# Kernel tuning notes

Measured on AMD Instinct MI355X. Metric: run time of the kernel, lower is better.

The kernel has to match this reference:

```python
import jax, jax.numpy as jnp
import numpy as np

B, L, D, NL, VOCAB = 2, 8192, 512, 8, 32
FFT_LEN = 2 * L  # causal linear conv via zero-padded FFT


def layernorm(x, g, b, eps=1e-5):
    mu = jnp.mean(x, axis=-1, keepdims=True)
    var = jnp.var(x, axis=-1, keepdims=True)
    return (x - mu) * jax.lax.rsqrt(var + eps) * g + b


def fftconv(v, h, bias):
    # v: [B, d, L], h: [d, L] long implicit filter, bias: [d] skip (the Hyena 'D' term)
    vf = jnp.fft.rfft(v, n=FFT_LEN)
    hf = jnp.fft.rfft(h, n=FFT_LEN)
    y = jnp.fft.irfft(vf * hf[None], n=FFT_LEN)[..., :L]
    return y + v * bias[:, None]


def short_conv(p, w, b):
    # causal depthwise conv, kernel size 3: p [B, C, L], w [C, 3], b [C]
    pp = jnp.pad(p, ((0, 0), (0, 0), (2, 0)))
    out = jax.lax.conv_general_dilated(pp, w[:, None, :], (1,), 'VALID',
                                       feature_group_count=p.shape[1])
    return out + b[None, :, None]


def setup_inputs() -> dict:
    key = jax.random.key(0)
    ks = jax.random.split(key, 12)
    rn = lambda k, sh, s: jax.random.normal(k, sh, jnp.float32) * s
    d = D
    return {
        'input_ids': jax.random.randint(ks[0], (B, L), 0, VOCAB),
        'emb': rn(ks[1], (VOCAB, d), 0.02),
        'ln1_g': jnp.ones((NL, d)), 'ln1_b': jnp.zeros((NL, d)),
        'Win': rn(ks[2], (NL, d, 3 * d), d ** -0.5), 'bin_': jnp.zeros((NL, 3 * d)),
        'convw': rn(ks[3], (NL, 3 * d, 3), 3 ** -0.5), 'convb': jnp.zeros((NL, 3 * d)),
        'h': rn(ks[4], (NL, d, L), L ** -0.5),  # implicit long filter, materialized
        'Db': rn(ks[5], (NL, d), 1.0),
        'Wout': rn(ks[6], (NL, d, d), d ** -0.5), 'bout': jnp.zeros((NL, d)),
        'ln2_g': jnp.ones((NL, d)), 'ln2_b': jnp.zeros((NL, d)),
        'W1': rn(ks[7], (NL, d, 4 * d), d ** -0.5), 'b1': jnp.zeros((NL, 4 * d)),
        'W2': rn(ks[8], (NL, 4 * d, d), (4 * d) ** -0.5), 'b2': jnp.zeros((NL, d)),
        'lnf_g': jnp.ones((d,)), 'lnf_b': jnp.zeros((d,)),
    }


def reference(input_ids, emb, ln1_g, ln1_b, Win, bin_, convw, convb, h, Db,
              Wout, bout, ln2_g, ln2_b, W1, b1, W2, b2, lnf_g, lnf_b):
    u = emb[input_ids]  # [B, L, d]
    for l in range(NL):  # structural loop over layers
        z = layernorm(u, ln1_g[l], ln1_b[l])
        p = (jnp.einsum('bld,de->ble', z, Win[l]) + bin_[l]).transpose(0, 2, 1)  # [B,3d,L]
        p = short_conv(p, convw[l], convb[l])
        x2, x1, v = jnp.split(p, 3, axis=1)  # each [B, d, L]
        v = fftconv(v * x1, h[l], Db[l])     # gate then FFT long conv (order-2 Hyena)
        y = (v * x2).transpose(0, 2, 1)      # output gate -> [B, L, d]
        u = u + jnp.einsum('bld,de->ble', y, Wout[l]) + bout[l]
        z = layernorm(u, ln2_g[l], ln2_b[l])
        hmid = jax.nn.gelu(jnp.einsum('bld,df->blf', z, W1[l]) + b1[l])
        u = u + jnp.einsum('blf,fd->bld', hmid, W2[l]) + b2[l]
    return layernorm(u, lnf_g, lnf_b)  # last_hidden_state [B, L, d]
```

## Files before the change

### kernel.cpp

```cpp
#include <hip/hip_runtime.h>
#include <hip/hip_bf16.h>
#include <math.h>

#define BB 2
#define LL 8192
#define DD 512
#define NLAYER 8
#define TD 1536
#define HD 2048
#define NFFT 16384
#define NHALF 8192
#define BLD (BB*LL*DD)
#define BLH ((size_t)BB*LL*HD)

typedef unsigned short u16;
typedef unsigned int   u32;
typedef __bf16 bf16x8 __attribute__((ext_vector_type(8)));
typedef float  f32x4  __attribute__((ext_vector_type(4)));

__device__ __forceinline__ u16 f2bf(float f) {
    union { float f; u32 u; } v; v.f = f;
    u32 r = v.u + 0x7FFF + ((v.u >> 16) & 1);
    return (u16)(r >> 16);
}
__device__ __forceinline__ float bf2f(u16 h) {
    union { u32 u; float f; } v; v.u = (u32)h << 16; return v.f;
}

__device__ __forceinline__ void async_g2l_16(const u16* g, u16* l) {
    __builtin_amdgcn_global_load_lds(
        (const __attribute__((address_space(1))) void*)g,
        (__attribute__((address_space(3))) void*)l,
        16, 0, 0);
}

__device__ __forceinline__ float2 cmul(float2 a, float2 b) {
    return make_float2(a.x * b.x - a.y * b.y, a.x * b.y + a.y * b.x);
}
__device__ __forceinline__ float2 cmulc(float2 a, float2 b) {
    return make_float2(a.x * b.x + a.y * b.y, a.y * b.x - a.x * b.y);
}
__device__ __forceinline__ float2 cadd(float2 a, float2 b) {
    return make_float2(a.x + b.x, a.y + b.y);
}
__device__ __forceinline__ float2 csub(float2 a, float2 b) {
    return make_float2(a.x - b.x, a.y - b.y);
}
__device__ __forceinline__ int drev12(int m) {
    return ((m & 3) << 10) | (((m >> 2) & 3) << 8) | (((m >> 4) & 3) << 6) |
           (((m >> 6) & 3) << 4) | (((m >> 8) & 3) << 2) | ((m >> 10) & 3);
}
__device__ __forceinline__ int perm8k(int k) {
    return ((k & 1) << 12) + drev12(k >> 1);
}

__global__ void twiddle_kernel(float* twf) {
    int k = blockIdx.x * 256 + threadIdx.x;
    if (k < NFFT) {
        double ang = -2.0 * M_PI * (double)k / (double)NFFT;
        twf[2 * k]     = (float)cos(ang);
        twf[2 * k + 1] = (float)sin(ang);
    }
}

__global__ void embed_kernel(const int* __restrict__ ids,
                             const float* __restrict__ emb,
                             float* __restrict__ u) {
    int i = blockIdx.x * 256 + threadIdx.x;
    if (i < BLD) {
        int row = i >> 9;
        int d   = i & (DD - 1);
        u[i] = emb[ids[row] * DD + d];
    }
}

__global__ __launch_bounds__(256)
void wprep_kernel(const float* __restrict__ W, u16* __restrict__ WtH,
                  u16* __restrict__ WtL, int K, int N, long srcStride, long dstStride) {
    __shared__ float t[64][65];
    const float* src = W + (size_t)blockIdx.z * srcStride;
    u16* dsth = WtH + (size_t)blockIdx.z * dstStride;
    u16* dstl = WtL + (size_t)blockIdx.z * dstStride;
    int n0 = blockIdx.x * 64, k0 = blockIdx.y * 64;
    int tc = threadIdx.x & 63, tr = threadIdx.x >> 6;
    for (int r = tr; r < 64; r += 4)
        t[r][tc] = src[(size_t)(k0 + r) * N + n0 + tc];
    __syncthreads();
    for (int r = tr; r < 64; r += 4) {
        float v = t[tc][r];
        u16 h = f2bf(v);
        dsth[(size_t)(n0 + r) * K + k0 + tc] = h;
        dstl[(size_t)(n0 + r) * K + k0 + tc] = f2bf(v - bf2f(h));
    }
}

template<int MODE>
__global__ __launch_bounds__(128)
void ln_kernel(const float* __restrict__ x, void* __restrict__ out,
               void* __restrict__ outL,
               const float* __restrict__ g, const float* __restrict__ b) {
    int row = blockIdx.x;
    const float4* xr = (const float4*)(x + (size_t)row * DD);
    int t = threadIdx.x;
    float4 v = xr[t];
    float s  = v.x + v.y + v.z + v.w;
    float ss = v.x * v.x + v.y * v.y + v.z * v.z + v.w * v.w;
    for (int off = 32; off; off >>= 1) {
        s  += __shfl_down(s, off);
        ss += __shfl_down(ss, off);
    }
    __shared__ float sm[4];
    if ((t & 63) == 0) { sm[(t >> 6) * 2] = s; sm[(t >> 6) * 2 + 1] = ss; }
    __syncthreads();
    float S = sm[0] + sm[2], SS = sm[1] + sm[3];
    float mu  = S * (1.0f / DD);
    float var = SS * (1.0f / DD) - mu * mu;
    float rs  = rsqrtf(var + 1e-5f);
    float4 gg = ((const float4*)g)[t];
    float4 bb = ((const float4*)b)[t];
    float o[4];
    o[0] = (v.x - mu) * rs * gg.x + bb.x;
    o[1] = (v.y - mu) * rs * gg.y + bb.y;
    o[2] = (v.z - mu) * rs * gg.z + bb.z;
    o[3] = (v.w - mu) * rs * gg.w + bb.w;
    if (MODE == 1) {
        u16 h[4], lo[4];
#pragma unroll
        for (int i = 0; i < 4; i++) {
            h[i]  = f2bf(o[i]);
            lo[i] = f2bf(o[i] - bf2f(h[i]));
        }
        uint2 ph, pl;
        ph.x = (u32)h[0] | ((u32)h[1] << 16);  ph.y = (u32)h[2] | ((u32)h[3] << 16);
        pl.x = (u32)lo[0] | ((u32)lo[1] << 16); pl.y = (u32)lo[2] | ((u32)lo[3] << 16);
        ((uint2*)((u16*)out  + (size_t)row * DD))[t] = ph;
        ((uint2*)((u16*)outL + (size_t)row * DD))[t] = pl;
    } else {
        float4 of = {o[0], o[1], o[2], o[3]};
        ((float4*)((float*)out + (size_t)row * DD))[t] = of;
    }
}

__device__ __forceinline__ float gelu_f(float x) {
    float x3 = x * x * x;
    float t  = tanhf(0.79788456080286541f * (x + 0.044715f * x3));
    return 0.5f * x * (1.0f + t);
}

template<int OUT, bool GELU, int PASSES>
__global__ __launch_bounds__(256)
void mfma_gemm3(const u16* __restrict__ Ah, const u16* __restrict__ Al,
                const u16* __restrict__ Bh, const u16* __restrict__ Bl,
                const float* __restrict__ bias,
                float* __restrict__ Cf, u16* __restrict__ Ch, u16* __restrict__ Cl,
                int M, int N, int K) {
    __shared__ u16 AsH[128 * 32];
    __shared__ u16 AsL[128 * 32];
    __shared__ u16 BsH[128 * 32];
    __shared__ u16 BsL[(PASSES == 3) ? 128 * 32 : 8];
    int m0 = blockIdx.y * 128, n0 = blockIdx.x * 128;
    int tid = threadIdx.x;
    int w = tid >> 6, l = tid & 63;
    int wr = w >> 1, wc = w & 1;

    int ch0 = w * 2, ch1 = ch0 + 1;
    size_t offA0 = (size_t)(m0 + ch0 * 16 + (l >> 2)) * K + (l & 3) * 8;
    size_t offA1 = (size_t)(m0 + ch1 * 16 + (l >> 2)) * K + (l & 3) * 8;
    size_t offB0 = (size_t)(n0 + ch0 * 16 + (l >> 2)) * K + (l & 3) * 8;
    size_t offB1 = (size_t)(n0 + ch1 * 16 + (l >> 2)) * K + (l & 3) * 8;

    f32x4 acc[4][4] = {};
    int arow = wr * 64 + (l & 15);
    int brow = wc * 64 + (l & 15);
    int kc   = (l >> 4) * 8;

    for (int k0 = 0; k0 < K; k0 += 32) {
        async_g2l_16(Ah + offA0 + k0, &AsH[ch0 * 512]);
        async_g2l_16(Ah + offA1 + k0, &AsH[ch1 * 512]);
        async_g2l_16(Al + offA0 + k0, &AsL[ch0 * 512]);
        async_g2l_16(Al + offA1 + k0, &AsL[ch1 * 512]);
        async_g2l_16(Bh + offB0 + k0, &BsH[ch0 * 512]);
        async_g2l_16(Bh + offB1 + k0, &BsH[ch1 * 512]);
        if (PASSES == 3) {
            async_g2l_16(Bl + offB0 + k0, &BsL[ch0 * 512]);
            async_g2l_16(Bl + offB1 + k0, &BsL[ch1 * 512]);
        }
        __syncthreads();
        bf16x8 ah[4], al[4], bh[4], bl[4];
#pragma unroll
        for (int i = 0; i < 4; i++) {
            ah[i] = *(const bf16x8*)&AsH[(arow + i * 16) * 32 + kc];
            al[i] = *(const bf16x8*)&AsL[(arow + i * 16) * 32 + kc];
            bh[i] = *(const bf16x8*)&BsH[(brow + i * 16) * 32 + kc];
            if (PASSES == 3)
                bl[i] = *(const bf16x8*)&BsL[(brow + i * 16) * 32 + kc];
        }
#pragma unroll
        for (int mi = 0; mi < 4; mi++)
#pragma unroll
            for (int ni = 0; ni < 4; ni++) {
                acc[mi][ni] = __builtin_amdgcn_mfma_f32_16x16x32_bf16(
                    ah[mi], bh[ni], acc[mi][ni], 0, 0, 0);
                acc[mi][ni] = __builtin_amdgcn_mfma_f32_16x16x32_bf16(
                    al[mi], bh[ni], acc[mi][ni], 0, 0, 0);
                if (PASSES == 3)
                    acc[mi][ni] = __builtin_amdgcn_mfma_f32_16x16x32_bf16(
                        ah[mi], bl[ni], acc[mi][ni], 0, 0, 0);
            }
        __syncthreads();
    }

    int lr = l >> 4, lc = l & 15;
#pragma unroll
    for (int mi = 0; mi < 4; mi++) {
#pragma unroll
        for (int ni = 0; ni < 4; ni++) {
            int col = n0 + wc * 64 + ni * 16 + lc;
            float bv = bias[col];
            int rowb = m0 + wr * 64 + mi * 16 + lr * 4;
#pragma unroll
            for (int r = 0; r < 4; r++) {
                float v = acc[mi][ni][r] + bv;
                if (GELU) v = gelu_f(v);
                size_t off = (size_t)(rowb + r) * N + col;
                if (OUT == 0) {
                    Cf[off] = v;
                } else if (OUT == 1) {
                    u16 h = f2bf(v);
                    Ch[off] = h;
                    Cl[off] = f2bf(v - bf2f(h));
                } else {
                    Cf[off] += v;
                }
            }
        }
    }
}

__global__ __launch_bounds__(256)
void conv_gate_kernel(const float* __restrict__ p, const float* __restrict__ cw,
                      const float* __restrict__ cb, float* __restrict__ vg,
                      float* __restrict__ x2s) {
    __shared__ float tvg[64][65];
    __shared__ float tx2[64][65];
    int b = blockIdx.z, c0 = blockIdx.y * 64, l0 = blockIdx.x * 64;
    int tc = threadIdx.x & 63, tr = threadIdx.x >> 6;
    const float* pb = p + (size_t)b * LL * TD;
    int cx2 = c0 + tc;
    int cx1 = DD + c0 + tc;
    int cv  = 2 * DD + c0 + tc;
    float w20 = cw[cx2 * 3], w21 = cw[cx2 * 3 + 1], w22 = cw[cx2 * 3 + 2], bx2 = cb[cx2];
    float w10 = cw[cx1 * 3], w11 = cw[cx1 * 3 + 1], w12 = cw[cx1 * 3 + 2], bx1 = cb[cx1];
    float wv0 = cw[cv * 3],  wv1 = cw[cv * 3 + 1],  wv2 = cw[cv * 3 + 2],  bv  = cb[cv];
    for (int r = tr; r < 64; r += 4) {
        int l = l0 + r;
        size_t o0 = (size_t)l * TD;
        float p2a = (l >= 2) ? pb[o0 - 2 * TD + cx2] : 0.f;
        float p1a = (l >= 1) ? pb[o0 - TD + cx2] : 0.f;
        float p0a = pb[o0 + cx2];
        float p2b = (l >= 2) ? pb[o0 - 2 * TD + cx1] : 0.f;
        float p1b = (l >= 1) ? pb[o0 - TD + cx1] : 0.f;
        float p0b = pb[o0 + cx1];
        float p2c = (l >= 2) ? pb[o0 - 2 * TD + cv] : 0.f;
        float p1c = (l >= 1) ? pb[o0 - TD + cv] : 0.f;
        float p0c = pb[o0 + cv];
        float x2v = w20 * p2a + w21 * p1a + w22 * p0a + bx2;
        float x1v = w10 * p2b + w11 * p1b + w12 * p0b + bx1;
        float vv  = wv0 * p2c + wv1 * p1c + wv2 * p0c + bv;
        tx2[r][tc] = x2v;
        tvg[r][tc] = vv * x1v;
    }
    __syncthreads();
    for (int r = tr; r < 64; r += 4) {
        size_t o = ((size_t)b * DD + c0 + r) * LL + l0 + tc;
        vg[o]  = tvg[tc][r];
        x2s[o] = tx2[tc][r];
    }
}

__global__ __launch_bounds__(256)
void ytr_kernel(const float* __restrict__ yg, u16* __restrict__ yh,
                u16* __restrict__ yl) {
    __shared__ float t[64][65];
    int b = blockIdx.z, c0 = blockIdx.y * 64, l0 = blockIdx.x * 64;
    int tc = threadIdx.x & 63, tr = threadIdx.x >> 6;
    for (int r = tr; r < 64; r += 4)
        t[r][tc] = yg[((size_t)b * DD + c0 + r) * LL + l0 + tc];
    __syncthreads();
    for (int r = tr; r < 64; r += 4) {
        float v = t[tc][r];
        u16 h = f2bf(v);
        size_t o = ((size_t)(b * LL + l0 + r)) * DD + c0 + tc;
        yh[o] = h;
        yl[o] = f2bf(v - bf2f(h));
    }
}

__device__ __forceinline__ void fft8192_fwd(float2* ld, const float2* __restrict__ tw, int tid) {
    __syncthreads();
    for (int n = tid; n < 4096; n += 1024) {
        float2 a = ld[n], b = ld[n + 4096];
        ld[n] = cadd(a, b);
        float2 d = csub(a, b);
        ld[n + 4096] = n ? cmul(d, tw[2 * n]) : d;
    }
    for (int s = 0; s < 6; s++) {
        int lm = 12 - 2 * s, lq = lm - 2;
        int Q = 1 << lq;
        __syncthreads();
        for (int g = tid; g < 2048; g += 1024) {
            int half = g >> 10, gg = g & 1023;
            int j = gg & (Q - 1);
            int base = (half << 12) + ((gg >> lq) << lm) + j;
            float2 x0 = ld[base], x1 = ld[base + Q], x2 = ld[base + 2 * Q], x3 = ld[base + 3 * Q];
            float2 a = cadd(x0, x2), b = csub(x0, x2);
            float2 c = cadd(x1, x3), d = csub(x1, x3);
            float2 mid = make_float2(d.y, -d.x);
            float2 u0 = cadd(a, c);
            float2 u1 = cadd(b, mid);
            float2 u2 = csub(a, c);
            float2 u3 = csub(b, mid);
            int e = j << (2 * s);
            if (e) {
                u1 = cmul(u1, tw[4 * e]);
                u2 = cmul(u2, tw[8 * e]);
                u3 = cmul(u3, tw[12 * e]);
            }
            ld[base] = u0; ld[base + Q] = u1; ld[base + 2 * Q] = u2; ld[base + 3 * Q] = u3;
        }
    }
    __syncthreads();
}

__device__ __forceinline__ void fft8192_inv(float2* ld, const float2* __restrict__ tw, int tid) {
    for (int s = 5; s >= 0; s--) {
        int lm = 12 - 2 * s, lq = lm - 2;
        int Q = 1 << lq;
        __syncthreads();
        for (int g = tid; g < 2048; g += 1024) {
            int half = g >> 10, gg = g & 1023;
            int j = gg & (Q - 1);
            int base = (half << 12) + ((gg >> lq) << lm) + j;
            int e = j << (2 * s);
            float2 v0 = ld[base];
            float2 v1 = ld[base + Q], v2 = ld[base + 2 * Q], v3 = ld[base + 3 * Q];
            if (e) {
                v1 = cmulc(v1, tw[4 * e]);
                v2 = cmulc(v2, tw[8 * e]);
                v3 = cmulc(v3, tw[12 * e]);
            }
            float2 a = cadd(v0, v2), b = csub(v0, v2);
            float2 c = cadd(v1, v3), d = csub(v1, v3);
            float2 id = make_float2(-d.y, d.x);
            ld[base]         = cadd(a, c);
            ld[base + Q]     = cadd(b, id);
            ld[base + 2 * Q] = csub(a, c);
            ld[base + 3 * Q] = csub(b, id);
        }
    }
    __syncthreads();
    for (int n = tid; n < 4096; n += 1024) {
        float2 a = ld[n];
        float2 b = ld[n + 4096];
        if (n) b = cmulc(b, tw[2 * n]);
        ld[n] = cadd(a, b);
        ld[n + 4096] = csub(a, b);
    }
    __syncthreads();
}

__global__ __launch_bounds__(1024, 8)
void hf_kernel(const float* __restrict__ h, float2* __restrict__ HfA,
               float2* __restrict__ HfB, const float* __restrict__ twf) {
    __shared__ float2 ld[NHALF];
    int c = blockIdx.x;
    const float2* hp = (const float2*)(h + (size_t)c * LL);
    const float2* tw = (const float2*)twf;
    int tid = threadIdx.x;
    for (int n = tid; n < 4096; n += 1024) ld[n] = hp[n];
    for (int n = 4096 + tid; n < NHALF; n += 1024) ld[n] = make_float2(0.f, 0.f);
    fft8192_fwd(ld, tw, tid);
    float2* oa = HfA + (size_t)c * NHALF;
    float2* ob = HfB + (size_t)c * NHALF;
    for (int k = tid; k <= 4096; k += 1024) {
        int kc = (NHALF - k) & (NHALF - 1);
        int p = perm8k(k), pc = perm8k(kc);
        float2 A = ld[p], B = ld[pc];
        float2 E = make_float2(0.5f * (A.x + B.x), 0.5f * (A.y - B.y));
        float2 O = make_float2(0.5f * (A.y + B.y), -0.5f * (A.x - B.x));
        float2 t = tw[k];
        float2 tO = cmul(t, O);
        float2 X1 = cadd(E, tO);
        float2 X2 = csub(E, tO);
        oa[k] = X1;
        ob[k] = X2;
        if (kc != k) {
            oa[kc] = make_float2(X2.x, -X2.y);
            ob[kc] = make_float2(X1.x, -X1.y);
        }
    }
}

__global__ __launch_bounds__(1024, 8)
void fftconv_kernel(const float* __restrict__ vg, const float* __restrict__ x2s,
                    const float2* __restrict__ HfA, const float2* __restrict__ HfB,
                    const float* __restrict__ Db, const float* __restrict__ twf,
                    float* __restrict__ yg) {
    __shared__ float2 ld[NHALF];
    int bc = blockIdx.x;
    int c  = bc & (DD - 1);
    const float2* vp  = (const float2*)(vg  + (size_t)bc * LL);
    const float2* x2p = (const float2*)(x2s + (size_t)bc * LL);
    float2*       op  = (float2*)(yg + (size_t)bc * LL);
    const float2* tw = (const float2*)twf;
    int tid = threadIdx.x;
    for (int n = tid; n < 4096; n += 1024) ld[n] = vp[n];
    for (int n = 4096 + tid; n < NHALF; n += 1024) ld[n] = make_float2(0.f, 0.f);
    fft8192_fwd(ld, tw, tid);
    const float2* Ha = HfA + (size_t)c * NHALF;
    const float2* Hb = HfB + (size_t)c * NHALF;
    for (int k = tid; k <= 4096; k += 1024) {
        int kc = (NHALF - k) & (NHALF - 1);
        int p = perm8k(k), pc = perm8k(kc);
        float2 A = ld[p], B = ld[pc];
        float2 E = make_float2(0.5f * (A.x + B.x), 0.5f * (A.y - B.y));
        float2 O = make_float2(0.5f * (A.y + B.y), -0.5f * (A.x - B.x));
        float2 t = tw[k];
        float2 tO = cmul(t, O);
        float2 X1 = cadd(E, tO);
        float2 X2 = csub(E, tO);
        float2 Y1 = cmul(X1, Ha[k]);
        float2 Y2 = cmul(X2, Hb[k]);
        float2 S  = make_float2(0.5f * (Y1.x + Y2.x), 0.5f * (Y1.y + Y2.y));
        float2 Dd = make_float2(0.5f * (Y1.x - Y2.x), 0.5f * (Y1.y - Y2.y));
        ld[p] = cadd(S, cmul(make_float2(t.y, t.x), Dd));
        if (kc != k) {
            float2 X1c = make_float2(X2.x, -X2.y);
            float2 X2c = make_float2(X1.x, -X1.y);
            float2 Y1c = cmul(X1c, Ha[kc]);
            float2 Y2c = cmul(X2c, Hb[kc]);
            float2 Sc = make_float2(0.5f * (Y1c.x + Y2c.x), 0.5f * (Y1c.y + Y2c.y));
            float2 Dc = make_float2(0.5f * (Y1c.x - Y2c.x), 0.5f * (Y1c.y - Y2c.y));
            ld[pc] = cadd(Sc, cmul(make_float2(t.y, -t.x), Dc));
        }
    }
    fft8192_inv(ld, tw, tid);
    float db = Db[c];
    const float inv = 1.0f / (float)NHALF;
    for (int n = tid; n < 4096; n += 1024) {
        float2 w  = ld[n];
        float2 vv = vp[n];
        float2 xx = x2p[n];
        float y0 = w.x * inv + vv.x * db;
        float y1 = w.y * inv + vv.y * db;
        op[n] = make_float2(y0 * xx.x, y1 * xx.y);
    }
}

extern "C" void kernel_launch(void* const* d_in, const int* in_sizes, int n_in,
                              void* d_out, int out_size, void* d_ws, size_t ws_size,
                              hipStream_t stream) {
    const int*   ids   = (const int*)  d_in[0];
    const float* emb   = (const float*)d_in[1];
    const float* ln1_g = (const float*)d_in[2];
    const float* ln1_b = (const float*)d_in[3];
    const float* Win   = (const float*)d_in[4];
    const float* bin_  = (const float*)d_in[5];
    const float* convw = (const float*)d_in[6];
    const float* convb = (const float*)d_in[7];
    const float* hflt  = (const float*)d_in[8];
    const float* Db    = (const float*)d_in[9];
    const float* Wout  = (const float*)d_in[10];
    const float* bout  = (const float*)d_in[11];
    const float* ln2_g = (const float*)d_in[12];
    const float* ln2_b = (const float*)d_in[13];
    const float* W1    = (const float*)d_in[14];
    const float* b1    = (const float*)d_in[15];
    const float* W2    = (const float*)d_in[16];
    const float* b2    = (const float*)d_in[17];
    const float* lnf_g = (const float*)d_in[18];
    const float* lnf_b = (const float*)d_in[19];

    char* p_ = (char*)d_ws;
    auto alloc = [&](size_t bytes) {
        char* r = p_; p_ += (bytes + 255) & ~(size_t)255; return r;
    };
    float* u   = (float*)alloc((size_t)BLD * 4);
    u16* zh    = (u16*)  alloc((size_t)BLD * 2);
    u16* zl    = (u16*)  alloc((size_t)BLD * 2);
    char* uni  = alloc(2 * BLH * 2);
    float* pf  = (float*)uni;
    float* yg  = (float*)uni;
    u16* hmh   = (u16*)uni;
    u16* hml   = hmh + BLH;
    float* vg  = (float*)alloc((size_t)BLD * 4);
    float* x2s = (float*)alloc((size_t)BLD * 4);
    u16* yh    = (u16*)  alloc((size_t)BLD * 2);
    u16* yl    = (u16*)  alloc((size_t)BLD * 2);
    float2* HfA = (float2*)alloc((size_t)DD * NHALF * 8);
    float2* HfB = (float2*)alloc((size_t)DD * NHALF * 8);
    float* tw  = (float*)alloc((size_t)2 * NFFT * 4);
    u16* WtInH = (u16*)alloc((size_t)NLAYER * TD * DD * 2);
    u16* WtInL = (u16*)alloc((size_t)NLAYER * TD * DD * 2);
    u16* WtOutH= (u16*)alloc((size_t)NLAYER * DD * DD * 2);
    u16* WtOutL= (u16*)alloc((size_t)NLAYER * DD * DD * 2);
    u16* Wt1H  = (u16*)alloc((size_t)NLAYER * DD * HD * 2);
    u16* Wt1L  = (u16*)alloc((size_t)NLAYER * DD * HD * 2);
    u16* Wt2H  = (u16*)alloc((size_t)NLAYER * HD * DD * 2);
    u16* Wt2L  = (u16*)alloc((size_t)NLAYER * HD * DD * 2);

    twiddle_kernel<<<(NFFT + 255) / 256, 256, 0, stream>>>(tw);
    embed_kernel<<<(BLD + 255) / 256, 256, 0, stream>>>(ids, emb, u);
    wprep_kernel<<<dim3(TD / 64, DD / 64, NLAYER), 256, 0, stream>>>(
        Win, WtInH, WtInL, DD, TD, (long)DD * TD, (long)TD * DD);
    wprep_kernel<<<dim3(DD / 64, DD / 64, NLAYER), 256, 0, stream>>>(
        Wout, WtOutH, WtOutL, DD, DD, (long)DD * DD, (long)DD * DD);
    wprep_kernel<<<dim3(HD / 64, DD / 64, NLAYER), 256, 0, stream>>>(
        W1, Wt1H, Wt1L, DD, HD, (long)DD * HD, (long)DD * HD);
    wprep_kernel<<<dim3(DD / 64, HD / 64, NLAYER), 256, 0, stream>>>(
        W2, Wt2H, Wt2L, HD, DD, (long)HD * DD, (long)HD * DD);

    for (int l = 0; l < NLAYER; l++) {
        ln_kernel<1><<<BB * LL, 128, 0, stream>>>(u, zh, zl,
            ln1_g + l * DD, ln1_b + l * DD);

        mfma_gemm3<0, false, 3><<<dim3(TD / 128, (BB * LL) / 128), 256, 0, stream>>>(
            zh, zl, WtInH + (size_t)l * TD * DD, WtInL + (size_t)l * TD * DD,
            bin_ + (size_t)l * TD, pf, nullptr, nullptr, BB * LL, TD, DD);

        conv_gate_kernel<<<dim3(LL / 64, DD / 64, BB), 256, 0, stream>>>(
            pf, convw + (size_t)l * TD * 3, convb + (size_t)l * TD, vg, x2s);

        hf_kernel<<<DD, 1024, 0, stream>>>(hflt + (size_t)l * DD * LL, HfA, HfB, tw);

        fftconv_kernel<<<BB * DD, 1024, 0, stream>>>(
            vg, x2s, HfA, HfB, Db + (size_t)l * DD, tw, yg);

        ytr_kernel<<<dim3(LL / 64, DD / 64, BB), 256, 0, stream>>>(yg, yh, yl);

        mfma_gemm3<2, false, 2><<<dim3(DD / 128, (BB * LL) / 128), 256, 0, stream>>>(
            yh, yl, WtOutH + (size_t)l * DD * DD, WtOutL + (size_t)l * DD * DD,
            bout + (size_t)l * DD, u, nullptr, nullptr, BB * LL, DD, DD);

        ln_kernel<1><<<BB * LL, 128, 0, stream>>>(u, zh, zl,
            ln2_g + l * DD, ln2_b + l * DD);

        mfma_gemm3<1, true, 2><<<dim3(HD / 128, (BB * LL) / 128), 256, 0, stream>>>(
            zh, zl, Wt1H + (size_t)l * DD * HD, Wt1L + (size_t)l * DD * HD,
            b1 + (size_t)l * HD, nullptr, hmh, hml, BB * LL, HD, DD);

        mfma_gemm3<2, false, 2><<<dim3(DD / 128, (BB * LL) / 128), 256, 0, stream>>>(
            hmh, hml, Wt2H + (size_t)l * HD * DD, Wt2L + (size_t)l * HD * DD,
            b2 + (size_t)l * DD, u, nullptr, nullptr, BB * LL, DD, HD);
    }

    ln_kernel<0><<<BB * LL, 128, 0, stream>>>(u, (float*)d_out, nullptr, lnf_g, lnf_b);
}
```

Baseline: 5.376 ms.

## Swizzle FFT shared-memory indices, halve filter spectrum storage, keep v in registers

Result: faster. 4.988 ms (-7.2%).

```diff
diff --git a/kernel.cpp b/kernel.cpp
--- a/kernel.cpp
+++ b/kernel.cpp
@@ -10,6 +10,7 @@
 #define HD 2048
 #define NFFT 16384
 #define NHALF 8192
+#define HSTR 4160
 #define BLD (BB*LL*DD)
 #define BLH ((size_t)BB*LL*HD)
 
@@ -53,6 +54,10 @@
 __device__ __forceinline__ int perm8k(int k) {
     return ((k & 1) << 12) + drev12(k >> 1);
 }
+__device__ __forceinline__ int swz(int i) {
+    return i ^ (((i >> 4) ^ (i >> 8)) & 15);
+}
+#define LDX(arr, i) arr[swz(i)]
 
 __global__ void twiddle_kernel(float* twf) {
     int k = blockIdx.x * 256 + threadIdx.x;
@@ -299,10 +304,10 @@
 __device__ __forceinline__ void fft8192_fwd(float2* ld, const float2* __restrict__ tw, int tid) {
     __syncthreads();
     for (int n = tid; n < 4096; n += 1024) {
-        float2 a = ld[n], b = ld[n + 4096];
-        ld[n] = cadd(a, b);
+        float2 a = LDX(ld, n), b = LDX(ld, n + 4096);
+        LDX(ld, n) = cadd(a, b);
         float2 d = csub(a, b);
-        ld[n + 4096] = n ? cmul(d, tw[2 * n]) : d;
+        LDX(ld, n + 4096) = n ? cmul(d, tw[2 * n]) : d;
     }
     for (int s = 0; s < 6; s++) {
         int lm = 12 - 2 * s, lq = lm - 2;
@@ -312,7 +317,8 @@
             int half = g >> 10, gg = g & 1023;
             int j = gg & (Q - 1);
             int base = (half << 12) + ((gg >> lq) << lm) + j;
-            float2 x0 = ld[base], x1 = ld[base + Q], x2 = ld[base + 2 * Q], x3 = ld[base + 3 * Q];
+            float2 x0 = LDX(ld, base), x1 = LDX(ld, base + Q);
+            float2 x2 = LDX(ld, base + 2 * Q), x3 = LDX(ld, base + 3 * Q);
             float2 a = cadd(x0, x2), b = csub(x0, x2);
             float2 c = cadd(x1, x3), d = csub(x1, x3);
             float2 mid = make_float2(d.y, -d.x);
@@ -326,7 +332,8 @@
                 u2 = cmul(u2, tw[8 * e]);
                 u3 = cmul(u3, tw[12 * e]);
             }
-            ld[base] = u0; ld[base + Q] = u1; ld[base + 2 * Q] = u2; ld[base + 3 * Q] = u3;
+            LDX(ld, base) = u0; LDX(ld, base + Q) = u1;
+            LDX(ld, base + 2 * Q) = u2; LDX(ld, base + 3 * Q) = u3;
         }
     }
     __syncthreads();
@@ -342,8 +349,8 @@
             int j = gg & (Q - 1);
             int base = (half << 12) + ((gg >> lq) << lm) + j;
             int e = j << (2 * s);
-            float2 v0 = ld[base];
-            float2 v1 = ld[base + Q], v2 = ld[base + 2 * Q], v3 = ld[base + 3 * Q];
+            float2 v0 = LDX(ld, base);
+            float2 v1 = LDX(ld, base + Q), v2 = LDX(ld, base + 2 * Q), v3 = LDX(ld, base + 3 * Q);
             if (e) {
                 v1 = cmulc(v1, tw[4 * e]);
                 v2 = cmulc(v2, tw[8 * e]);
@@ -352,19 +359,19 @@
             float2 a = cadd(v0, v2), b = csub(v0, v2);
             float2 c = cadd(v1, v3), d = csub(v1, v3);
             float2 id = make_float2(-d.y, d.x);
-            ld[base]         = cadd(a, c);
-            ld[base + Q]     = cadd(b, id);
-            ld[base + 2 * Q] = csub(a, c);
-            ld[base + 3 * Q] = csub(b, id);
+            LDX(ld, base)         = cadd(a, c);
+            LDX(ld, base + Q)     = cadd(b, id);
+            LDX(ld, base + 2 * Q) = csub(a, c);
+            LDX(ld, base + 3 * Q) = csub(b, id);
         }
     }
     __syncthreads();
     for (int n = tid; n < 4096; n += 1024) {
-        float2 a = ld[n];
-        float2 b = ld[n + 4096];
+        float2 a = LDX(ld, n);
+        float2 b = LDX(ld, n + 4096);
         if (n) b = cmulc(b, tw[2 * n]);
-        ld[n] = cadd(a, b);
-        ld[n + 4096] = csub(a, b);
+        LDX(ld, n) = cadd(a, b);
+        LDX(ld, n + 4096) = csub(a, b);
     }
     __syncthreads();
 }
@@ -377,27 +384,21 @@
     const float2* hp = (const float2*)(h + (size_t)c * LL);
     const float2* tw = (const float2*)twf;
     int tid = threadIdx.x;
-    for (int n = tid; n < 4096; n += 1024) ld[n] = hp[n];
-    for (int n = 4096 + tid; n < NHALF; n += 1024) ld[n] = make_float2(0.f, 0.f);
+    for (int n = tid; n < 4096; n += 1024) LDX(ld, n) = hp[n];
+    for (int n = 4096 + tid; n < NHALF; n += 1024) LDX(ld, n) = make_float2(0.f, 0.f);
     fft8192_fwd(ld, tw, tid);
-    float2* oa = HfA + (size_t)c * NHALF;
-    float2* ob = HfB + (size_t)c * NHALF;
+    float2* oa = HfA + (size_t)c * HSTR;
+    float2* ob = HfB + (size_t)c * HSTR;
     for (int k = tid; k <= 4096; k += 1024) {
         int kc = (NHALF - k) & (NHALF - 1);
         int p = perm8k(k), pc = perm8k(kc);
-        float2 A = ld[p], B = ld[pc];
+        float2 A = LDX(ld, p), B = LDX(ld, pc);
         float2 E = make_float2(0.5f * (A.x + B.x), 0.5f * (A.y - B.y));
         float2 O = make_float2(0.5f * (A.y + B.y), -0.5f * (A.x - B.x));
         float2 t = tw[k];
         float2 tO = cmul(t, O);
-        float2 X1 = cadd(E, tO);
-        float2 X2 = csub(E, tO);
-        oa[k] = X1;
-        ob[k] = X2;
-        if (kc != k) {
-            oa[kc] = make_float2(X2.x, -X2.y);
-            ob[kc] = make_float2(X1.x, -X1.y);
-        }
+        oa[k] = cadd(E, tO);
+        ob[k] = csub(E, tO);
     }
 }
 
@@ -414,45 +415,54 @@
     float2*       op  = (float2*)(yg + (size_t)bc * LL);
     const float2* tw = (const float2*)twf;
     int tid = threadIdx.x;
-    for (int n = tid; n < 4096; n += 1024) ld[n] = vp[n];
-    for (int n = 4096 + tid; n < NHALF; n += 1024) ld[n] = make_float2(0.f, 0.f);
+    float2 vv[4];
+#pragma unroll
+    for (int q = 0; q < 4; q++) {
+        int n = tid + q * 1024;
+        vv[q] = vp[n];
+        LDX(ld, n) = vv[q];
+    }
+#pragma unroll
+    for (int q = 0; q < 4; q++) LDX(ld, tid + 4096 + q * 1024) = make_float2(0.f, 0.f);
     fft8192_fwd(ld, tw, tid);
-    const float2* Ha = HfA + (size_t)c * NHALF;
-    const float2* Hb = HfB + (size_t)c * NHALF;
+    const float2* Ha = HfA + (size_t)c * HSTR;
+    const float2* Hb = HfB + (size_t)c * HSTR;
     for (int k = tid; k <= 4096; k += 1024) {
         int kc = (NHALF - k) & (NHALF - 1);
         int p = perm8k(k), pc = perm8k(kc);
-        float2 A = ld[p], B = ld[pc];
+        float2 A = LDX(ld, p), B = LDX(ld, pc);
         float2 E = make_float2(0.5f * (A.x + B.x), 0.5f * (A.y - B.y));
         float2 O = make_float2(0.5f * (A.y + B.y), -0.5f * (A.x - B.x));
         float2 t = tw[k];
         float2 tO = cmul(t, O);
         float2 X1 = cadd(E, tO);
         float2 X2 = csub(E, tO);
-        float2 Y1 = cmul(X1, Ha[k]);
-        float2 Y2 = cmul(X2, Hb[k]);
+        float2 Hak = Ha[k], Hbk = Hb[k];
+        float2 Y1 = cmul(X1, Hak);
+        float2 Y2 = cmul(X2, Hbk);
         float2 S  = make_float2(0.5f * (Y1.x + Y2.x), 0.5f * (Y1.y + Y2.y));
         float2 Dd = make_float2(0.5f * (Y1.x - Y2.x), 0.5f * (Y1.y - Y2.y));
-        ld[p] = cadd(S, cmul(make_float2(t.y, t.x), Dd));
+        LDX(ld, p) = cadd(S, cmul(make_float2(t.y, t.x), Dd));
         if (kc != k) {
             float2 X1c = make_float2(X2.x, -X2.y);
             float2 X2c = make_float2(X1.x, -X1.y);
-            float2 Y1c = cmul(X1c, Ha[kc]);
-            float2 Y2c = cmul(X2c, Hb[kc]);
+            float2 Y1c = cmulc(X1c, Hbk);
+            float2 Y2c = cmulc(X2c, Hak);
             float2 Sc = make_float2(0.5f * (Y1c.x + Y2c.x), 0.5f * (Y1c.y + Y2c.y));
             float2 Dc = make_float2(0.5f * (Y1c.x - Y2c.x), 0.5f * (Y1c.y - Y2c.y));
-            ld[pc] = cadd(Sc, cmul(make_float2(t.y, -t.x), Dc));
+            LDX(ld, pc) = cadd(Sc, cmul(make_float2(t.y, -t.x), Dc));
         }
     }
     fft8192_inv(ld, tw, tid);
     float db = Db[c];
     const float inv = 1.0f / (float)NHALF;
-    for (int n = tid; n < 4096; n += 1024) {
-        float2 w  = ld[n];
-        float2 vv = vp[n];
+#pragma unroll
+    for (int q = 0; q < 4; q++) {
+        int n = tid + q * 1024;
+        float2 w  = LDX(ld, n);
         float2 xx = x2p[n];
-        float y0 = w.x * inv + vv.x * db;
-        float y1 = w.y * inv + vv.y * db;
+        float y0 = w.x * inv + vv[q].x * db;
+        float y1 = w.y * inv + vv[q].y * db;
         op[n] = make_float2(y0 * xx.x, y1 * xx.y);
     }
 }
@@ -497,8 +507,8 @@
     float* x2s = (float*)alloc((size_t)BLD * 4);
     u16* yh    = (u16*)  alloc((size_t)BLD * 2);
     u16* yl    = (u16*)  alloc((size_t)BLD * 2);
-    float2* HfA = (float2*)alloc((size_t)DD * NHALF * 8);
-    float2* HfB = (float2*)alloc((size_t)DD * NHALF * 8);
+    float2* HfA = (float2*)alloc((size_t)DD * HSTR * 8);
+    float2* HfB = (float2*)alloc((size_t)DD * HSTR * 8);
     float* tw  = (float*)alloc((size_t)2 * NFFT * 4);
     u16* WtInH = (u16*)alloc((size_t)NLAYER * TD * DD * 2);
     u16* WtInL = (u16*)alloc((size_t)NLAYER * TD * DD * 2);
```
